# Kernel optimization log

Measured on AMD Instinct MI355X. Metric: run time of the kernel, lower is better.

## Reference

```python
import jax, jax.numpy as jnp
import numpy as np

N_NODES = 50000
N_EDGES = 1600000
IN_DIM = 128
HID = 128


def setup_inputs() -> dict:
    key = jax.random.key(0)
    ks = jax.random.split(key, 12)
    s = 1.0 / np.sqrt(HID)
    return {
        "x": jax.random.normal(ks[0], (N_NODES, IN_DIM), jnp.float32),
        "src": jax.random.randint(ks[1], (N_EDGES,), 0, N_NODES, jnp.int32),
        "dst": jax.random.randint(ks[2], (N_EDGES,), 0, N_NODES, jnp.int32),
        "W0": jax.random.normal(ks[3], (IN_DIM, HID), jnp.float32) * s,
        "b0": jnp.zeros((HID,), jnp.float32),
        "W1": jax.random.normal(ks[4], (HID, HID), jnp.float32) * s,
        "b1": jnp.zeros((HID,), jnp.float32),
        "W2": jax.random.normal(ks[5], (HID, HID), jnp.float32) * s,
        "b2": jnp.zeros((HID,), jnp.float32),
        "w_pg": jax.random.normal(ks[6], (HID, 1), jnp.float32) * s,
        "b_pg": jnp.zeros((1,), jnp.float32),
        "w_pd": jax.random.normal(ks[7], (HID, 1), jnp.float32) * s,
        "b_pd": jnp.zeros((1,), jnp.float32),
        "w_v": jax.random.normal(ks[8], (HID, 1), jnp.float32) * s,
        "b_v": jnp.zeros((1,), jnp.float32),
    }


def _gcn_layer(h, src, dst, W, b):
    # DGL-style GCN: gather source features along edges, sum-scatter to dst,
    # then per-node Linear + ReLU.  agg: [N, d]
    agg = jax.ops.segment_sum(h[src], dst, num_segments=N_NODES)
    return jax.nn.relu(agg @ W + b)


def reference(x, src, dst, W0, b0, W1, b1, W2, b2, w_pg, b_pg, w_pd, b_pd, w_v, b_v):
    h = _gcn_layer(x, src, dst, W0, b0)
    h = _gcn_layer(h, src, dst, W1, b1)
    h = _gcn_layer(h, src, dst, W2, b2)
    mN = jnp.mean(h, axis=0, keepdims=True)          # dgl.mean_nodes -> [1, HID]
    v = mN @ w_v + b_v                                # [1, 1]
    pi_graph = h @ w_pg + b_pg                        # [N, 1]
    pi_done = mN @ w_pd + b_pd                        # [1, 1]
    pi = jnp.concatenate([pi_graph, pi_done], axis=0)  # [N+1, 1]
    return (pi, v)
```

## Files before the change

### kernel.cpp

```cpp
#include <hip/hip_runtime.h>
#include <hip/hip_bf16.h>


#define HID 128
#define NBLK 256
#define BSH 6
#define SCAN_CHUNK 1024
#define CS_BLOCKS 256

typedef __attribute__((ext_vector_type(8))) short short8;
typedef __attribute__((ext_vector_type(4))) float f32x4;

__device__ __forceinline__ unsigned short f2bf(float f) {
    unsigned int u = __float_as_uint(f);
    unsigned int r = (u + 0x7fffu + ((u >> 16) & 1u)) >> 16;
    return (unsigned short)r;
}
__device__ __forceinline__ float bf2f(unsigned short u) {
    return __uint_as_float(((unsigned int)u) << 16);
}

__global__ __launch_bounds__(256) void f32_to_bf16_kernel(
        const float4* __restrict__ in, ushort4* __restrict__ out, int n4) {
    for (int i = blockIdx.x * blockDim.x + threadIdx.x; i < n4; i += gridDim.x * blockDim.x) {
        float4 v = in[i];
        ushort4 o;
        o.x = f2bf(v.x); o.y = f2bf(v.y); o.z = f2bf(v.z); o.w = f2bf(v.w);
        out[i] = o;
    }
}

__global__ __launch_bounds__(256) void pack_w_kernel(
        const float* __restrict__ W, unsigned short* __restrict__ packw) {
    for (int j = blockIdx.x * blockDim.x + threadIdx.x; j < 16384; j += gridDim.x * blockDim.x) {
        int i = j & 7, lane = (j >> 3) & 63, kk = (j >> 9) & 3, c = (j >> 11) & 7;
        int k = kk * 32 + (lane >> 4) * 8 + i;
        int col = c * 16 + (lane & 15);
        packw[j] = f2bf(W[k * 128 + col]);
    }
}

__global__ __launch_bounds__(256) void bhist_kernel(const int* __restrict__ dst,
        int* __restrict__ tbl, int ne, int nb, int epb) {
    __shared__ int lcnt[1024];
    const int k = blockIdx.x, t = threadIdx.x;
    for (int b = t; b < nb; b += 256) lcnt[b] = 0;
    __syncthreads();
    const int beg = k * epb, end = min(ne, beg + epb);
    for (int j = beg + t; j < end; j += 256)
        atomicAdd(&lcnt[dst[j] >> BSH], 1);
    __syncthreads();
    for (int b = t; b < nb; b += 256) tbl[b * NBLK + k] = lcnt[b];
}

__global__ __launch_bounds__(256) void scan_p1_kernel(const int* __restrict__ tbl,
        int* __restrict__ bsum, int sz) {
    __shared__ int sh[256];
    const int g = blockIdx.x, t = threadIdx.x;
    const int base = g * SCAN_CHUNK + t * 4;
    int s = 0;
    if (base + 3 < sz) {
        int4 v = *(const int4*)(tbl + base);
        s = v.x + v.y + v.z + v.w;
    } else {
        for (int i = 0; i < 4; ++i) if (base + i < sz) s += tbl[base + i];
    }
    sh[t] = s;
    __syncthreads();
    for (int off = 128; off > 0; off >>= 1) {
        if (t < off) sh[t] += sh[t + off];
        __syncthreads();
    }
    if (t == 0) bsum[g] = sh[0];
}

__global__ __launch_bounds__(256) void scan_p2_kernel(int* __restrict__ bsum, int ng) {
    __shared__ int sh[256];
    const int t = threadIdx.x;
    int v = (t < ng) ? bsum[t] : 0;
    sh[t] = v;
    __syncthreads();
    for (int off = 1; off < 256; off <<= 1) {
        int a = sh[t];
        int b = (t >= off) ? sh[t - off] : 0;
        __syncthreads();
        sh[t] = a + b;
        __syncthreads();
    }
    if (t < ng) bsum[t] = sh[t] - v;
}

__global__ __launch_bounds__(256) void scan_p3_kernel(int* __restrict__ tbl,
        const int* __restrict__ bsum, int sz) {
    __shared__ int sh[256];
    const int g = blockIdx.x, t = threadIdx.x;
    const int base = g * SCAN_CHUNK + t * 4;
    int4 v = make_int4(0, 0, 0, 0);
    if (base + 3 < sz) {
        v = *(const int4*)(tbl + base);
    } else {
        if (base + 0 < sz) v.x = tbl[base + 0];
        if (base + 1 < sz) v.y = tbl[base + 1];
        if (base + 2 < sz) v.z = tbl[base + 2];
    }
    int s = v.x + v.y + v.z + v.w;
    sh[t] = s;
    __syncthreads();
    for (int off = 1; off < 256; off <<= 1) {
        int a = sh[t];
        int b = (t >= off) ? sh[t - off] : 0;
        __syncthreads();
        sh[t] = a + b;
        __syncthreads();
    }
    int pre = bsum[g] + sh[t] - s;
    int o0 = pre, o1 = pre + v.x, o2 = o1 + v.y, o3 = o2 + v.z;
    if (base + 3 < sz) {
        *(int4*)(tbl + base) = make_int4(o0, o1, o2, o3);
    } else {
        if (base + 0 < sz) tbl[base + 0] = o0;
        if (base + 1 < sz) tbl[base + 1] = o1;
        if (base + 2 < sz) tbl[base + 2] = o2;
    }
}

__global__ __launch_bounds__(256) void bucket_scatter_kernel(
        const int* __restrict__ src, const int* __restrict__ dst,
        const int* __restrict__ tbl, int* __restrict__ pairs,
        int ne, int nb, int epb) {
    __shared__ int cur[1024];
    const int k = blockIdx.x, t = threadIdx.x;
    for (int b = t; b < nb; b += 256) cur[b] = tbl[b * NBLK + k];
    __syncthreads();
    const int beg = k * epb, end = min(ne, beg + epb);
    for (int j = beg + t; j < end; j += 256) {
        int d = dst[j];
        int pos = atomicAdd(&cur[d >> BSH], 1);
        pairs[pos] = (src[j] << BSH) | (d & 63);
    }
}

__global__ __launch_bounds__(256) void fine_scatter_kernel(
        const int* __restrict__ pairs, const int* __restrict__ tbl,
        int* __restrict__ row_ptr, int* __restrict__ eidx,
        int ne, int nb, int n) {
    __shared__ int cnt[64], cur[64];
    const int b = blockIdx.x, t = threadIdx.x;
    const int node0 = b << BSH;
    if (t < 64) cnt[t] = 0;
    __syncthreads();
    const int beg = tbl[b * NBLK];
    const int end = (b == nb - 1) ? ne : tbl[(b + 1) * NBLK];
    for (int j = beg + t; j < end; j += 256) atomicAdd(&cnt[pairs[j] & 63], 1);
    __syncthreads();
    if (t == 0) {
        int run = beg;
        #pragma unroll
        for (int i = 0; i < 64; ++i) { cur[i] = run; run += cnt[i]; }
    }
    __syncthreads();
    if (t < 64 && node0 + t < n) row_ptr[node0 + t] = cur[t];
    if (b == nb - 1 && t == 0) row_ptr[n] = ne;
    __syncthreads();
    for (int j = beg + t; j < end; j += 256) {
        int v = pairs[j];
        int pos = atomicAdd(&cur[v & 63], 1);
        eidx[pos] = v >> BSH;
    }
}

__global__ __launch_bounds__(256) void aggregate_bf_kernel(
        const uint2* __restrict__ xb, const int* __restrict__ row_ptr,
        const int* __restrict__ eidx, uint2* __restrict__ aggb, int n) {
    int g = (int)((blockIdx.x * blockDim.x + threadIdx.x) >> 5);
    int lane = threadIdx.x & 31;
    if (g >= n) return;
    const int beg = row_ptr[g], end = row_ptr[g + 1];
    float4 acc = make_float4(0.f, 0.f, 0.f, 0.f);
    int e = beg;
    for (; e + 4 <= end; e += 4) {
        int s0 = eidx[e], s1 = eidx[e + 1], s2 = eidx[e + 2], s3 = eidx[e + 3];
        uint2 v0 = xb[(size_t)s0 * 32 + lane];
        uint2 v1 = xb[(size_t)s1 * 32 + lane];
        uint2 v2 = xb[(size_t)s2 * 32 + lane];
        uint2 v3 = xb[(size_t)s3 * 32 + lane];
        acc.x += __uint_as_float(v0.x << 16); acc.y += __uint_as_float(v0.x & 0xffff0000u);
        acc.z += __uint_as_float(v0.y << 16); acc.w += __uint_as_float(v0.y & 0xffff0000u);
        acc.x += __uint_as_float(v1.x << 16); acc.y += __uint_as_float(v1.x & 0xffff0000u);
        acc.z += __uint_as_float(v1.y << 16); acc.w += __uint_as_float(v1.y & 0xffff0000u);
        acc.x += __uint_as_float(v2.x << 16); acc.y += __uint_as_float(v2.x & 0xffff0000u);
        acc.z += __uint_as_float(v2.y << 16); acc.w += __uint_as_float(v2.y & 0xffff0000u);
        acc.x += __uint_as_float(v3.x << 16); acc.y += __uint_as_float(v3.x & 0xffff0000u);
        acc.z += __uint_as_float(v3.y << 16); acc.w += __uint_as_float(v3.y & 0xffff0000u);
    }
    for (; e < end; ++e) {
        int s = eidx[e];
        uint2 v = xb[(size_t)s * 32 + lane];
        acc.x += __uint_as_float(v.x << 16); acc.y += __uint_as_float(v.x & 0xffff0000u);
        acc.z += __uint_as_float(v.y << 16); acc.w += __uint_as_float(v.y & 0xffff0000u);
    }
    uint2 o;
    o.x = (unsigned)f2bf(acc.x) | ((unsigned)f2bf(acc.y) << 16);
    o.y = (unsigned)f2bf(acc.z) | ((unsigned)f2bf(acc.w) << 16);
    aggb[(size_t)g * 32 + lane] = o;
}

__global__ __launch_bounds__(256) void gemm_mfma_kernel(
        const short* __restrict__ A, const short* __restrict__ packw,
        const float* __restrict__ bias, unsigned short* __restrict__ out, int M) {
    const int w = threadIdx.x >> 6, l = threadIdx.x & 63;
    const int m = l & 15, hi = l >> 4;
    const int row0 = blockIdx.x * 64 + w * 16;
    const int arow = row0 + m;
    const bool valid = arow < M;

    short8 afrag[4];
    #pragma unroll
    for (int kk = 0; kk < 4; ++kk) {
        if (valid)
            afrag[kk] = *(const short8*)(A + (size_t)arow * 128 + kk * 32 + hi * 8);
        else
            afrag[kk] = short8{0, 0, 0, 0, 0, 0, 0, 0};
    }

    f32x4 acc[8] = {};
    #pragma unroll
    for (int kk = 0; kk < 4; ++kk) {
        #pragma unroll
        for (int c = 0; c < 8; ++c) {
            short8 bfrag = *(const short8*)(packw + ((size_t)(c * 4 + kk) * 64 + l) * 8);
            acc[c] = __builtin_amdgcn_mfma_f32_16x16x32_bf16(afrag[kk], bfrag, acc[c], 0, 0, 0);
        }
    }

    #pragma unroll
    for (int c = 0; c < 8; ++c) {
        float bcol = bias[c * 16 + m];
        #pragma unroll
        for (int r = 0; r < 4; ++r) {
            int row = row0 + hi * 4 + r;
            if (row < M)
                out[(size_t)row * 128 + c * 16 + m] = f2bf(fmaxf(acc[c][r] + bcol, 0.f));
        }
    }
}

__global__ __launch_bounds__(256) void colsum_part_kernel(
        const uint2* __restrict__ hb, float* __restrict__ part, int n) {
    __shared__ float sh[8][32][4];
    const int t = threadIdx.x;
    const int cg = t & 31, rl = t >> 5;
    float4 acc = make_float4(0.f, 0.f, 0.f, 0.f);
    for (int r = blockIdx.x * 8 + rl; r < n; r += gridDim.x * 8) {
        uint2 v = hb[(size_t)r * 32 + cg];
        acc.x += __uint_as_float(v.x << 16);
        acc.y += __uint_as_float(v.x & 0xffff0000u);
        acc.z += __uint_as_float(v.y << 16);
        acc.w += __uint_as_float(v.y & 0xffff0000u);
    }
    sh[rl][cg][0] = acc.x; sh[rl][cg][1] = acc.y;
    sh[rl][cg][2] = acc.z; sh[rl][cg][3] = acc.w;
    __syncthreads();
    for (int off = 4; off > 0; off >>= 1) {
        if (rl < off) {
            #pragma unroll
            for (int i = 0; i < 4; ++i)
                sh[rl][cg][i] += sh[rl + off][cg][i];
        }
        __syncthreads();
    }
    if (rl == 0) {
        #pragma unroll
        for (int i = 0; i < 4; ++i)
            part[blockIdx.x * 128 + cg * 4 + i] = sh[0][cg][i];
    }
}

__global__ __launch_bounds__(1024) void head_final_kernel(
        const float* __restrict__ part, int nparts,
        const float* __restrict__ w_v, const float* __restrict__ b_v,
        const float* __restrict__ w_pd, const float* __restrict__ b_pd,
        float* __restrict__ out, int n_nodes) {
    __shared__ float sh[32][128];
    __shared__ float sv[128], sd[128];
    const int t = threadIdx.x;
    const int d4 = t & 31, pg = t >> 5;
    float4 acc = make_float4(0.f, 0.f, 0.f, 0.f);
    for (int i = pg; i < nparts; i += 32) {
        float4 v = *(const float4*)(part + (size_t)i * 128 + d4 * 4);
        acc.x += v.x; acc.y += v.y; acc.z += v.z; acc.w += v.w;
    }
    *(float4*)&sh[pg][d4 * 4] = acc;
    __syncthreads();
    for (int off = 16; off > 0; off >>= 1) {
        if (pg < off) {
            float4 a = *(float4*)&sh[pg][d4 * 4];
            float4 b = *(float4*)&sh[pg + off][d4 * 4];
            a.x += b.x; a.y += b.y; a.z += b.z; a.w += b.w;
            *(float4*)&sh[pg][d4 * 4] = a;
        }
        __syncthreads();
    }
    if (t < 128) {
        float m = sh[0][t] / (float)n_nodes;
        sv[t] = m * w_v[t];
        sd[t] = m * w_pd[t];
    }
    __syncthreads();
    for (int off = 64; off > 0; off >>= 1) {
        if (t < off) { sv[t] += sv[t + off]; sd[t] += sd[t + off]; }
        __syncthreads();
    }
    if (t == 0) {
        out[n_nodes] = sd[0] + b_pd[0];
        out[n_nodes + 1] = sv[0] + b_v[0];
    }
}

__global__ __launch_bounds__(256) void pig_kernel(
        const unsigned short* __restrict__ h, const float* __restrict__ w_pg,
        const float* __restrict__ b_pg, float* __restrict__ out, int n) {
    int g = (int)((blockIdx.x * blockDim.x + threadIdx.x) >> 6);
    int l = threadIdx.x & 63;
    if (g >= n) return;
    float acc = bf2f(h[(size_t)g * 128 + l]) * w_pg[l] +
                bf2f(h[(size_t)g * 128 + 64 + l]) * w_pg[64 + l];
    #pragma unroll
    for (int off = 32; off > 0; off >>= 1) acc += __shfl_xor(acc, off);
    if (l == 0) out[g] = acc + b_pg[0];
}

static inline size_t align_up(size_t v, size_t a) { return (v + a - 1) & ~(a - 1); }

extern "C" void kernel_launch(void* const* d_in, const int* in_sizes, int n_in,
                              void* d_out, int out_size, void* d_ws, size_t ws_size,
                              hipStream_t stream) {
    const float* x    = (const float*)d_in[0];
    const int*   src  = (const int*)d_in[1];
    const int*   dst  = (const int*)d_in[2];
    const float* W0   = (const float*)d_in[3];
    const float* b0   = (const float*)d_in[4];
    const float* W1   = (const float*)d_in[5];
    const float* b1   = (const float*)d_in[6];
    const float* W2   = (const float*)d_in[7];
    const float* b2   = (const float*)d_in[8];
    const float* w_pg = (const float*)d_in[9];
    const float* b_pg = (const float*)d_in[10];
    const float* w_pd = (const float*)d_in[11];
    const float* b_pd = (const float*)d_in[12];
    const float* w_v  = (const float*)d_in[13];
    const float* b_v  = (const float*)d_in[14];
    float* out = (float*)d_out;

    const int NN = in_sizes[0] / HID;
    const int NE = in_sizes[1];
    const int NB = (NN + 63) >> BSH;
    const int SZ = NB * NBLK;
    const int EPB = (NE + NBLK - 1) / NBLK;
    const int NG = (SZ + SCAN_CHUNK - 1) / SCAN_CHUNK;

    char* w = (char*)d_ws;
    int* tbl      = (int*)w;            w += align_up((size_t)SZ * 4, 256);
    int* bsum     = (int*)w;            w += align_up((size_t)256 * 4, 256);
    int* row_ptr  = (int*)w;            w += align_up((size_t)(NN + 1) * 4, 256);
    int* eidx     = (int*)w;            w += align_up((size_t)NE * 4, 256);
    unsigned short* xb   = (unsigned short*)w; w += align_up((size_t)NN * HID * 2, 256);
    unsigned short* aggb = (unsigned short*)w; w += align_up((size_t)NN * HID * 2, 256);
    unsigned short* hb   = (unsigned short*)w; w += align_up((size_t)NN * HID * 2, 256);
    unsigned short* pw0  = (unsigned short*)w; w += align_up((size_t)16384 * 2, 256);
    unsigned short* pw1  = (unsigned short*)w; w += align_up((size_t)16384 * 2, 256);
    unsigned short* pw2  = (unsigned short*)w; w += align_up((size_t)16384 * 2, 256);
    float* part   = (float*)w;          w += align_up((size_t)CS_BLOCKS * 128 * 4, 256);
    int* pairs    = (int*)aggb;
    (void)ws_size; (void)n_in; (void)out_size;

    f32_to_bf16_kernel<<<2048, 256, 0, stream>>>((const float4*)x, (ushort4*)xb, NN * 32);
    pack_w_kernel<<<16, 256, 0, stream>>>(W0, pw0);
    pack_w_kernel<<<16, 256, 0, stream>>>(W1, pw1);
    pack_w_kernel<<<16, 256, 0, stream>>>(W2, pw2);

    bhist_kernel<<<NBLK, 256, 0, stream>>>(dst, tbl, NE, NB, EPB);
    scan_p1_kernel<<<NG, 256, 0, stream>>>(tbl, bsum, SZ);
    scan_p2_kernel<<<1, 256, 0, stream>>>(bsum, NG);
    scan_p3_kernel<<<NG, 256, 0, stream>>>(tbl, bsum, SZ);
    bucket_scatter_kernel<<<NBLK, 256, 0, stream>>>(src, dst, tbl, pairs, NE, NB, EPB);
    fine_scatter_kernel<<<NB, 256, 0, stream>>>(pairs, tbl, row_ptr, eidx, NE, NB, NN);

    const int agg_blocks = (NN * 32 + 255) / 256;
    const int gemm_blocks = (NN + 63) / 64;

    aggregate_bf_kernel<<<agg_blocks, 256, 0, stream>>>((const uint2*)xb, row_ptr, eidx,
                                                        (uint2*)aggb, NN);
    gemm_mfma_kernel<<<gemm_blocks, 256, 0, stream>>>((const short*)aggb, (const short*)pw0,
                                                      b0, hb, NN);
    aggregate_bf_kernel<<<agg_blocks, 256, 0, stream>>>((const uint2*)hb, row_ptr, eidx,
                                                        (uint2*)aggb, NN);
    gemm_mfma_kernel<<<gemm_blocks, 256, 0, stream>>>((const short*)aggb, (const short*)pw1,
                                                      b1, hb, NN);
    aggregate_bf_kernel<<<agg_blocks, 256, 0, stream>>>((const uint2*)hb, row_ptr, eidx,
                                                        (uint2*)aggb, NN);
    gemm_mfma_kernel<<<gemm_blocks, 256, 0, stream>>>((const short*)aggb, (const short*)pw2,
                                                      b2, hb, NN);

    colsum_part_kernel<<<CS_BLOCKS, 256, 0, stream>>>((const uint2*)hb, part, NN);
    head_final_kernel<<<1, 1024, 0, stream>>>(part, CS_BLOCKS, w_v, b_v, w_pd, b_pd, out, NN);
    pig_kernel<<<(NN * 64 + 255) / 256, 256, 0, stream>>>(hb, w_pg, b_pg, out, NN);
}
```

Baseline: 291.1 us.

## Fuse aggregation, GEMM and output heads into one per-layer kernel

Each GCN layer now gathers neighbour features into a shared-memory tile and runs the MFMA GEMM on it within the same block, so the aggregated matrix is never written to or read back from global memory. The last layer also computes the per-node policy logits and per-block column sums in its epilogue, which replaces the separate colsum and pig kernels. The three weight-packing launches become one. In exchange, each block now handles 64 nodes with 8 sequential rows per warp group, which lowers gather parallelism and may leave latency exposed, and it doubles the workspace buffers so layers can ping-pong.

```diff
diff --git a/kernel.cpp b/kernel.cpp
--- a/kernel.cpp
+++ b/kernel.cpp
@@ -6,15 +6,13 @@
 #define NBLK 256
 #define BSH 6
 #define SCAN_CHUNK 1024
-#define CS_BLOCKS 256
 
 typedef __attribute__((ext_vector_type(8))) short short8;
 typedef __attribute__((ext_vector_type(4))) float f32x4;
 
-__device__ __forceinline__ unsigned short f2bf(float f) {
+__device__ __forceinline__ unsigned int f2bf(float f) {
     unsigned int u = __float_as_uint(f);
-    unsigned int r = (u + 0x7fffu + ((u >> 16) & 1u)) >> 16;
-    return (unsigned short)r;
+    return (u + 0x7fffu + ((u >> 16) & 1u)) >> 16;
 }
 __device__ __forceinline__ float bf2f(unsigned short u) {
     return __uint_as_float(((unsigned int)u) << 16);
@@ -25,18 +23,23 @@
     for (int i = blockIdx.x * blockDim.x + threadIdx.x; i < n4; i += gridDim.x * blockDim.x) {
         float4 v = in[i];
         ushort4 o;
-        o.x = f2bf(v.x); o.y = f2bf(v.y); o.z = f2bf(v.z); o.w = f2bf(v.w);
+        o.x = (unsigned short)f2bf(v.x); o.y = (unsigned short)f2bf(v.y);
+        o.z = (unsigned short)f2bf(v.z); o.w = (unsigned short)f2bf(v.w);
         out[i] = o;
     }
 }
 
-__global__ __launch_bounds__(256) void pack_w_kernel(
-        const float* __restrict__ W, unsigned short* __restrict__ packw) {
-    for (int j = blockIdx.x * blockDim.x + threadIdx.x; j < 16384; j += gridDim.x * blockDim.x) {
-        int i = j & 7, lane = (j >> 3) & 63, kk = (j >> 9) & 3, c = (j >> 11) & 7;
+__global__ __launch_bounds__(256) void pack_w3_kernel(
+        const float* __restrict__ W0, const float* __restrict__ W1,
+        const float* __restrict__ W2, unsigned short* __restrict__ pw) {
+    for (int j = blockIdx.x * blockDim.x + threadIdx.x; j < 3 * 16384;
+         j += gridDim.x * blockDim.x) {
+        int jj = j & 16383, which = j >> 14;
+        const float* W = (which == 0) ? W0 : (which == 1) ? W1 : W2;
+        int i = jj & 7, lane = (jj >> 3) & 63, kk = (jj >> 9) & 3, c = (jj >> 11) & 7;
         int k = kk * 32 + (lane >> 4) * 8 + i;
         int col = c * 16 + (lane & 15);
-        packw[j] = f2bf(W[k * 128 + col]);
+        pw[j] = (unsigned short)f2bf(W[k * 128 + col]);
     }
 }
 
@@ -169,59 +172,64 @@
     }
 }
 
-__global__ __launch_bounds__(256) void aggregate_bf_kernel(
+__global__ __launch_bounds__(256) void layer_fused_kernel(
         const uint2* __restrict__ xb, const int* __restrict__ row_ptr,
-        const int* __restrict__ eidx, uint2* __restrict__ aggb, int n) {
-    int g = (int)((blockIdx.x * blockDim.x + threadIdx.x) >> 5);
-    int lane = threadIdx.x & 31;
-    if (g >= n) return;
-    const int beg = row_ptr[g], end = row_ptr[g + 1];
-    float4 acc = make_float4(0.f, 0.f, 0.f, 0.f);
-    int e = beg;
-    for (; e + 4 <= end; e += 4) {
-        int s0 = eidx[e], s1 = eidx[e + 1], s2 = eidx[e + 2], s3 = eidx[e + 3];
-        uint2 v0 = xb[(size_t)s0 * 32 + lane];
-        uint2 v1 = xb[(size_t)s1 * 32 + lane];
-        uint2 v2 = xb[(size_t)s2 * 32 + lane];
-        uint2 v3 = xb[(size_t)s3 * 32 + lane];
-        acc.x += __uint_as_float(v0.x << 16); acc.y += __uint_as_float(v0.x & 0xffff0000u);
-        acc.z += __uint_as_float(v0.y << 16); acc.w += __uint_as_float(v0.y & 0xffff0000u);
-        acc.x += __uint_as_float(v1.x << 16); acc.y += __uint_as_float(v1.x & 0xffff0000u);
-        acc.z += __uint_as_float(v1.y << 16); acc.w += __uint_as_float(v1.y & 0xffff0000u);
-        acc.x += __uint_as_float(v2.x << 16); acc.y += __uint_as_float(v2.x & 0xffff0000u);
-        acc.z += __uint_as_float(v2.y << 16); acc.w += __uint_as_float(v2.y & 0xffff0000u);
-        acc.x += __uint_as_float(v3.x << 16); acc.y += __uint_as_float(v3.x & 0xffff0000u);
-        acc.z += __uint_as_float(v3.y << 16); acc.w += __uint_as_float(v3.y & 0xffff0000u);
-    }
-    for (; e < end; ++e) {
-        int s = eidx[e];
-        uint2 v = xb[(size_t)s * 32 + lane];
-        acc.x += __uint_as_float(v.x << 16); acc.y += __uint_as_float(v.x & 0xffff0000u);
-        acc.z += __uint_as_float(v.y << 16); acc.w += __uint_as_float(v.y & 0xffff0000u);
-    }
-    uint2 o;
-    o.x = (unsigned)f2bf(acc.x) | ((unsigned)f2bf(acc.y) << 16);
-    o.y = (unsigned)f2bf(acc.z) | ((unsigned)f2bf(acc.w) << 16);
-    aggb[(size_t)g * 32 + lane] = o;
-}
-
-__global__ __launch_bounds__(256) void gemm_mfma_kernel(
-        const short* __restrict__ A, const short* __restrict__ packw,
-        const float* __restrict__ bias, unsigned short* __restrict__ out, int M) {
-    const int w = threadIdx.x >> 6, l = threadIdx.x & 63;
+        const int* __restrict__ eidx, const short* __restrict__ packw,
+        const float* __restrict__ bias, unsigned short* __restrict__ hb,
+        float* __restrict__ part, float* __restrict__ pig_out,
+        const float* __restrict__ w_pg, const float* __restrict__ b_pg,
+        int n) {
+    __shared__ unsigned short Ash[64][136];
+    __shared__ float colp[4][128];
+    const int t = threadIdx.x;
+
+    {
+        const int grp = t >> 5, lane = t & 31;
+        for (int i = 0; i < 8; ++i) {
+            const int r = grp * 8 + i;
+            const int g = blockIdx.x * 64 + r;
+            float4 acc = make_float4(0.f, 0.f, 0.f, 0.f);
+            if (g < n) {
+                const int beg = row_ptr[g], end = row_ptr[g + 1];
+                int e = beg;
+                for (; e + 4 <= end; e += 4) {
+                    int s0 = eidx[e], s1 = eidx[e + 1], s2 = eidx[e + 2], s3 = eidx[e + 3];
+                    uint2 v0 = xb[(size_t)s0 * 32 + lane];
+                    uint2 v1 = xb[(size_t)s1 * 32 + lane];
+                    uint2 v2 = xb[(size_t)s2 * 32 + lane];
+                    uint2 v3 = xb[(size_t)s3 * 32 + lane];
+                    acc.x += __uint_as_float(v0.x << 16); acc.y += __uint_as_float(v0.x & 0xffff0000u);
+                    acc.z += __uint_as_float(v0.y << 16); acc.w += __uint_as_float(v0.y & 0xffff0000u);
+                    acc.x += __uint_as_float(v1.x << 16); acc.y += __uint_as_float(v1.x & 0xffff0000u);
+                    acc.z += __uint_as_float(v1.y << 16); acc.w += __uint_as_float(v1.y & 0xffff0000u);
+                    acc.x += __uint_as_float(v2.x << 16); acc.y += __uint_as_float(v2.x & 0xffff0000u);
+                    acc.z += __uint_as_float(v2.y << 16); acc.w += __uint_as_float(v2.y & 0xffff0000u);
+                    acc.x += __uint_as_float(v3.x << 16); acc.y += __uint_as_float(v3.x & 0xffff0000u);
+                    acc.z += __uint_as_float(v3.y << 16); acc.w += __uint_as_float(v3.y & 0xffff0000u);
+                }
+                for (; e < end; ++e) {
+                    int s = eidx[e];
+                    uint2 v = xb[(size_t)s * 32 + lane];
+                    acc.x += __uint_as_float(v.x << 16); acc.y += __uint_as_float(v.x & 0xffff0000u);
+                    acc.z += __uint_as_float(v.y << 16); acc.w += __uint_as_float(v.y & 0xffff0000u);
+                }
+            }
+            uint2 o;
+            o.x = f2bf(acc.x) | (f2bf(acc.y) << 16);
+            o.y = f2bf(acc.z) | (f2bf(acc.w) << 16);
+            *(uint2*)&Ash[r][lane * 4] = o;
+        }
+    }
+    __syncthreads();
+
+    const int w = t >> 6, l = t & 63;
     const int m = l & 15, hi = l >> 4;
     const int row0 = blockIdx.x * 64 + w * 16;
-    const int arow = row0 + m;
-    const bool valid = arow < M;
 
     short8 afrag[4];
     #pragma unroll
-    for (int kk = 0; kk < 4; ++kk) {
-        if (valid)
-            afrag[kk] = *(const short8*)(A + (size_t)arow * 128 + kk * 32 + hi * 8);
-        else
-            afrag[kk] = short8{0, 0, 0, 0, 0, 0, 0, 0};
-    }
+    for (int kk = 0; kk < 4; ++kk)
+        afrag[kk] = *(const short8*)&Ash[w * 16 + m][kk * 32 + hi * 8];
 
     f32x4 acc[8] = {};
     #pragma unroll
@@ -233,46 +241,42 @@
         }
     }
 
+    float hvv[8][4];
     #pragma unroll
     for (int c = 0; c < 8; ++c) {
         float bcol = bias[c * 16 + m];
         #pragma unroll
         for (int r = 0; r < 4; ++r) {
             int row = row0 + hi * 4 + r;
-            if (row < M)
-                out[(size_t)row * 128 + c * 16 + m] = f2bf(fmaxf(acc[c][r] + bcol, 0.f));
-        }
-    }
-}
-
-__global__ __launch_bounds__(256) void colsum_part_kernel(
-        const uint2* __restrict__ hb, float* __restrict__ part, int n) {
-    __shared__ float sh[8][32][4];
-    const int t = threadIdx.x;
-    const int cg = t & 31, rl = t >> 5;
-    float4 acc = make_float4(0.f, 0.f, 0.f, 0.f);
-    for (int r = blockIdx.x * 8 + rl; r < n; r += gridDim.x * 8) {
-        uint2 v = hb[(size_t)r * 32 + cg];
-        acc.x += __uint_as_float(v.x << 16);
-        acc.y += __uint_as_float(v.x & 0xffff0000u);
-        acc.z += __uint_as_float(v.y << 16);
-        acc.w += __uint_as_float(v.y & 0xffff0000u);
-    }
-    sh[rl][cg][0] = acc.x; sh[rl][cg][1] = acc.y;
-    sh[rl][cg][2] = acc.z; sh[rl][cg][3] = acc.w;
-    __syncthreads();
-    for (int off = 4; off > 0; off >>= 1) {
-        if (rl < off) {
+            float hv = (row < n) ? fmaxf(acc[c][r] + bcol, 0.f) : 0.f;
+            hvv[c][r] = hv;
+            if (row < n)
+                hb[(size_t)row * 128 + c * 16 + m] = (unsigned short)f2bf(hv);
+        }
+    }
+
+    if (w_pg) {
+        #pragma unroll
+        for (int r = 0; r < 4; ++r) {
+            float p = 0.f;
             #pragma unroll
-            for (int i = 0; i < 4; ++i)
-                sh[rl][cg][i] += sh[rl + off][cg][i];
-        }
-        __syncthreads();
-    }
-    if (rl == 0) {
-        #pragma unroll
-        for (int i = 0; i < 4; ++i)
-            part[blockIdx.x * 128 + cg * 4 + i] = sh[0][cg][i];
+            for (int c = 0; c < 8; ++c) p += hvv[c][r] * w_pg[c * 16 + m];
+            #pragma unroll
+            for (int off = 1; off < 16; off <<= 1) p += __shfl_xor(p, off);
+            int row = row0 + hi * 4 + r;
+            if (m == 0 && row < n) pig_out[row] = p + b_pg[0];
+        }
+        #pragma unroll
+        for (int c = 0; c < 8; ++c) {
+            float v = hvv[c][0] + hvv[c][1] + hvv[c][2] + hvv[c][3];
+            v += __shfl_xor(v, 16);
+            v += __shfl_xor(v, 32);
+            if (hi == 0) colp[w][c * 16 + m] = v;
+        }
+        __syncthreads();
+        if (t < 128)
+            part[(size_t)blockIdx.x * 128 + t] =
+                colp[0][t] + colp[1][t] + colp[2][t] + colp[3][t];
     }
 }
 
@@ -302,9 +306,9 @@
         __syncthreads();
     }
     if (t < 128) {
-        float m = sh[0][t] / (float)n_nodes;
-        sv[t] = m * w_v[t];
-        sd[t] = m * w_pd[t];
+        float mm = sh[0][t] / (float)n_nodes;
+        sv[t] = mm * w_v[t];
+        sd[t] = mm * w_pd[t];
     }
     __syncthreads();
     for (int off = 64; off > 0; off >>= 1) {
@@ -315,19 +319,6 @@
         out[n_nodes] = sd[0] + b_pd[0];
         out[n_nodes + 1] = sv[0] + b_v[0];
     }
-}
-
-__global__ __launch_bounds__(256) void pig_kernel(
-        const unsigned short* __restrict__ h, const float* __restrict__ w_pg,
-        const float* __restrict__ b_pg, float* __restrict__ out, int n) {
-    int g = (int)((blockIdx.x * blockDim.x + threadIdx.x) >> 6);
-    int l = threadIdx.x & 63;
-    if (g >= n) return;
-    float acc = bf2f(h[(size_t)g * 128 + l]) * w_pg[l] +
-                bf2f(h[(size_t)g * 128 + 64 + l]) * w_pg[64 + l];
-    #pragma unroll
-    for (int off = 32; off > 0; off >>= 1) acc += __shfl_xor(acc, off);
-    if (l == 0) out[g] = acc + b_pg[0];
 }
 
 static inline size_t align_up(size_t v, size_t a) { return (v + a - 1) & ~(a - 1); }
@@ -358,26 +349,23 @@
     const int SZ = NB * NBLK;
     const int EPB = (NE + NBLK - 1) / NBLK;
     const int NG = (SZ + SCAN_CHUNK - 1) / SCAN_CHUNK;
+    const int LBLK = (NN + 63) / 64;
 
     char* w = (char*)d_ws;
     int* tbl      = (int*)w;            w += align_up((size_t)SZ * 4, 256);
     int* bsum     = (int*)w;            w += align_up((size_t)256 * 4, 256);
     int* row_ptr  = (int*)w;            w += align_up((size_t)(NN + 1) * 4, 256);
     int* eidx     = (int*)w;            w += align_up((size_t)NE * 4, 256);
-    unsigned short* xb   = (unsigned short*)w; w += align_up((size_t)NN * HID * 2, 256);
-    unsigned short* aggb = (unsigned short*)w; w += align_up((size_t)NN * HID * 2, 256);
-    unsigned short* hb   = (unsigned short*)w; w += align_up((size_t)NN * HID * 2, 256);
-    unsigned short* pw0  = (unsigned short*)w; w += align_up((size_t)16384 * 2, 256);
-    unsigned short* pw1  = (unsigned short*)w; w += align_up((size_t)16384 * 2, 256);
-    unsigned short* pw2  = (unsigned short*)w; w += align_up((size_t)16384 * 2, 256);
-    float* part   = (float*)w;          w += align_up((size_t)CS_BLOCKS * 128 * 4, 256);
-    int* pairs    = (int*)aggb;
+    unsigned short* xb = (unsigned short*)w; w += align_up((size_t)NN * HID * 2, 256);
+    unsigned short* hb = (unsigned short*)w; w += align_up((size_t)NN * HID * 2, 256);
+    unsigned short* hb2 = (unsigned short*)w; w += align_up((size_t)NN * HID * 2, 256);
+    unsigned short* pw = (unsigned short*)w; w += align_up((size_t)3 * 16384 * 2, 256);
+    float* part   = (float*)w;          w += align_up((size_t)LBLK * 128 * 4, 256);
+    int* pairs    = (int*)hb;
     (void)ws_size; (void)n_in; (void)out_size;
 
     f32_to_bf16_kernel<<<2048, 256, 0, stream>>>((const float4*)x, (ushort4*)xb, NN * 32);
-    pack_w_kernel<<<16, 256, 0, stream>>>(W0, pw0);
-    pack_w_kernel<<<16, 256, 0, stream>>>(W1, pw1);
-    pack_w_kernel<<<16, 256, 0, stream>>>(W2, pw2);
+    pack_w3_kernel<<<48, 256, 0, stream>>>(W0, W1, W2, pw);
 
     bhist_kernel<<<NBLK, 256, 0, stream>>>(dst, tbl, NE, NB, EPB);
     scan_p1_kernel<<<NG, 256, 0, stream>>>(tbl, bsum, SZ);
@@ -386,23 +374,15 @@
     bucket_scatter_kernel<<<NBLK, 256, 0, stream>>>(src, dst, tbl, pairs, NE, NB, EPB);
     fine_scatter_kernel<<<NB, 256, 0, stream>>>(pairs, tbl, row_ptr, eidx, NE, NB, NN);
 
-    const int agg_blocks = (NN * 32 + 255) / 256;
-    const int gemm_blocks = (NN + 63) / 64;
-
-    aggregate_bf_kernel<<<agg_blocks, 256, 0, stream>>>((const uint2*)xb, row_ptr, eidx,
-                                                        (uint2*)aggb, NN);
-    gemm_mfma_kernel<<<gemm_blocks, 256, 0, stream>>>((const short*)aggb, (const short*)pw0,
-                                                      b0, hb, NN);
-    aggregate_bf_kernel<<<agg_blocks, 256, 0, stream>>>((const uint2*)hb, row_ptr, eidx,
-                                                        (uint2*)aggb, NN);
-    gemm_mfma_kernel<<<gemm_blocks, 256, 0, stream>>>((const short*)aggb, (const short*)pw1,
-                                                      b1, hb, NN);
-    aggregate_bf_kernel<<<agg_blocks, 256, 0, stream>>>((const uint2*)hb, row_ptr, eidx,
-                                                        (uint2*)aggb, NN);
-    gemm_mfma_kernel<<<gemm_blocks, 256, 0, stream>>>((const short*)aggb, (const short*)pw2,
-                                                      b2, hb, NN);
-
-    colsum_part_kernel<<<CS_BLOCKS, 256, 0, stream>>>((const uint2*)hb, part, NN);
-    head_final_kernel<<<1, 1024, 0, stream>>>(part, CS_BLOCKS, w_v, b_v, w_pd, b_pd, out, NN);
-    pig_kernel<<<(NN * 64 + 255) / 256, 256, 0, stream>>>(hb, w_pg, b_pg, out, NN);
-}
+    layer_fused_kernel<<<LBLK, 256, 0, stream>>>(
+        (const uint2*)xb, row_ptr, eidx, (const short*)pw, b0, hb2,
+        nullptr, nullptr, nullptr, nullptr, NN);
+    layer_fused_kernel<<<LBLK, 256, 0, stream>>>(
+        (const uint2*)hb2, row_ptr, eidx, (const short*)(pw + 16384), b1, hb,
+        nullptr, nullptr, nullptr, nullptr, NN);
+    layer_fused_kernel<<<LBLK, 256, 0, stream>>>(
+        (const uint2*)hb, row_ptr, eidx, (const short*)(pw + 32768), b2, hb2,
+        part, out, w_pg, b_pg, NN);
+
+    head_final_kernel<<<1, 1024, 0, stream>>>(part, LBLK, w_v, b_v, w_pd, b_pd, out, NN);
+}
```

Measured after the change: 314.4 us. +8.0%, slower.
